# Optimization experiments

Measured on AMD Instinct MI355X. Metric: run time of the kernel, lower is better.

The kernel has to match this reference:

```python
import jax, jax.numpy as jnp
import numpy as np


def _pano_affinity():
    # Faithful port of get_pano_affinity(): 3 rings of 12 views, 3x3 Gaussian
    # blur (cv2 ksize=3 sigma=0 => sigma=0.8), BORDER_TRANSPARENT (borders kept),
    # diagonal reset to 1; zeros replaced by 0.01 as done in __init__.
    p = np.eye(36, dtype=np.float64)
    for v in range(12):  # top ring
        p[v, v + 12] = 1
        l = (v - 1) % 12
        r = (v + 1) % 12
        p[v, l] = 1; p[v, l + 12] = 1
        p[v, r] = 1; p[v, r + 12] = 1
    for v in range(12, 24):  # middle ring
        p[v, v + 12] = 1; p[v, v - 12] = 1
        l = (v - 13) % 12 + 12
        r = (v - 11) % 12 + 12
        p[v, l] = 1; p[v, l + 12] = 1; p[v, l - 12] = 1
        p[v, r] = 1; p[v, r + 12] = 1; p[v, r - 12] = 1
    for v in range(24, 36):  # bottom ring
        p[v, v - 12] = 1
        l = (v - 25) % 12 + 24
        r = (v - 23) % 12 + 24
        p[v, l] = 1; p[v, l - 12] = 1
        p[v, r] = 1; p[v, r - 12] = 1
    assert np.sum(p - p.T) == 0
    kern = np.exp(-np.array([-1.0, 0.0, 1.0]) ** 2 / (2 * 0.8 ** 2))
    kern /= kern.sum()
    a, b = kern[0], kern[1]
    t = a * p[:, :-2] + b * p[:, 1:-1] + a * p[:, 2:]
    t2 = a * t[:-2, :] + b * t[1:-1, :] + a * t[2:, :]
    out = p.copy()
    out[1:-1, 1:-1] = t2  # transparent border: edge pixels unblurred
    out[np.eye(36, dtype=bool)] = 1.0
    out[out == 0] = 0.01
    return out.astype(np.float32)


def _ln(x, g, b):
    mu = jnp.mean(x, -1, keepdims=True)
    v = jnp.mean(jnp.square(x - mu), -1, keepdims=True)
    return (x - mu) * jax.lax.rsqrt(v + 1e-5) * g + b


def setup_inputs() -> dict:
    key = jax.random.key(0)
    ks = jax.random.split(key, 12)
    B, L, V, D, KD, KV, Q, H = 128, 36, 36, 512, 300, 112, 36, 512
    s = 0.02
    return {
        'h': jax.random.normal(ks[0], (B, Q), jnp.float32),
        'context': jax.random.normal(ks[1], (B, L, V, D), jnp.float32),
        'teacher_action_view_ids': jax.random.randint(ks[2], (B,), 0, 36),
        'detect_feats': jax.random.normal(ks[3], (B, L, KD), jnp.float32),
        'knowledge_vector': jax.random.normal(ks[4], (B, L, KV), jnp.float32),
        'pano_a': jnp.asarray(_pano_affinity()),
        'W_q': jax.random.normal(ks[5], (Q, Q), jnp.float32) * s,
        'W_k': jax.random.normal(ks[6], (Q, D + KD), jnp.float32) * s,
        'gru_Wih': jax.random.normal(ks[7], (3 * Q, D + KV), jnp.float32) * s,
        'gru_Whh': jax.random.normal(ks[8], (3 * Q, Q), jnp.float32) * s,
        'gru_bih': jnp.zeros((3 * Q,), jnp.float32),
        'gru_bhh': jnp.zeros((3 * Q,), jnp.float32),
        'ln_slots_g': jnp.ones((Q,), jnp.float32),
        'ln_slots_b': jnp.zeros((Q,), jnp.float32),
        'ln_ff_g': jnp.ones((Q,), jnp.float32),
        'ln_ff_b': jnp.zeros((Q,), jnp.float32),
        'mlp_W1': jax.random.normal(ks[9], (H, Q), jnp.float32) * s,
        'mlp_b1': jnp.zeros((H,), jnp.float32),
        'mlp_W2': jax.random.normal(ks[10], (Q, H), jnp.float32) * s,
        'mlp_b2': jnp.zeros((Q,), jnp.float32),
    }


def reference(h, context, teacher_action_view_ids, detect_feats, knowledge_vector,
              pano_a, W_q, W_k, gru_Wih, gru_Whh, gru_bih, gru_bhh,
              ln_slots_g, ln_slots_b, ln_ff_g, ln_ff_b,
              mlp_W1, mlp_b1, mlp_W2, mlp_b2):
    B, L, V, D = context.shape
    Q = pano_a.shape[0]  # 36
    scale = Q ** -0.5
    iters = 3
    slots = jnp.broadcast_to(pano_a, (B, Q, Q))
    # context_know = cat(context, detect_feats broadcast over 36 views)
    ck = jnp.concatenate(
        [context, jnp.broadcast_to(detect_feats[:, :, None, :], (B, L, V, detect_feats.shape[-1]))], axis=-1)
    k = jnp.einsum('bljc,qc->bljq', ck, W_k)  # [B,L,36,Q]
    attn_ws = []
    for _ in range(iters):
        slots_prev = slots
        q = jnp.einsum('bie,qe->biq', _ln(slots, ln_slots_g, ln_slots_b), W_q)  # [B,Q,Q]
        dots = jnp.einsum('bid,bkjd->bkj', q, k) * scale  # i summed out, as in source
        attn = jax.nn.softmax(dots, axis=-1)  # softmax over views
        attn_ws.append(attn)
        updates = jnp.einsum('bkjd,bij->bid', context, attn)  # [B,L,D]
        x = jnp.concatenate([updates, knowledge_vector], axis=-1).reshape(-1, D + knowledge_vector.shape[-1])
        hp = slots_prev.reshape(-1, Q)
        # torch.nn.GRUCell (gate order r, z, n)
        gx = x @ gru_Wih.T + gru_bih
        gh = hp @ gru_Whh.T + gru_bhh
        xr, xz, xn = jnp.split(gx, 3, axis=-1)
        hr, hz, hn = jnp.split(gh, 3, axis=-1)
        r = jax.nn.sigmoid(xr + hr)
        z = jax.nn.sigmoid(xz + hz)
        n = jnp.tanh(xn + r * hn)
        gnew = ((1.0 - z) * n + z * hp).reshape(B, -1, Q)
        ff = _ln(gnew, ln_ff_g, ln_ff_b)
        gnew = gnew + (jax.nn.relu(ff @ mlp_W1.T + mlp_b1) @ mlp_W2.T + mlp_b2)
        slots = gnew
    return slots, jnp.stack(attn_ws, 0)
```

## Files before the change

### kernel.cpp

```cpp
#include <hip/hip_runtime.h>

namespace {
constexpr int Bc = 128, Lc = 36, Vc = 36, Dc = 512, KDc = 300, KVc = 112, Qc = 36, Hc = 512;
constexpr int ROWS = Bc * Lc * Vc;
constexpr int BLn  = Bc * Lc;
constexpr int SLOT = Bc * Qc * Qc;
constexpr float SCALE = 1.0f / 6.0f;
}

__device__ __forceinline__ float wave_sum(float v) {
  #pragma unroll
  for (int off = 32; off > 0; off >>= 1) v += __shfl_xor(v, off, 64);
  return v;
}
__device__ __forceinline__ float wave_max(float v) {
  #pragma unroll
  for (int off = 32; off > 0; off >>= 1) v = fmaxf(v, __shfl_xor(v, off, 64));
  return v;
}
__device__ __forceinline__ float sigmoidf_(float x) { return 1.f / (1.f + __expf(-x)); }
__device__ __forceinline__ float dot4_(float4 a, float4 b) {
  return fmaf(a.x, b.x, fmaf(a.y, b.y, fmaf(a.z, b.z, a.w * b.w)));
}

__global__ __launch_bounds__(256) void csum_kernel(const float* __restrict__ ctx, float* __restrict__ csum) {
  int tid = blockIdx.x * 256 + threadIdx.x;
  int b  = tid / (Vc * Dc);
  int jd = tid % (Vc * Dc);
  const float* p = ctx + (size_t)b * Lc * Vc * Dc + jd;
  float s = 0.f;
  #pragma unroll
  for (int l = 0; l < Lc; ++l) s += p[(size_t)l * (Vc * Dc)];
  csum[tid] = s;
}

__global__ void kd_kernel(const float* __restrict__ det, const float* __restrict__ Wk,
                          float* __restrict__ kd) {
  __shared__ float ds[KDc];
  int bl = blockIdx.x; int t = threadIdx.x;
  for (int c = t; c < KDc; c += 64) ds[c] = det[(size_t)bl * KDc + c];
  __syncthreads();
  if (t < Qc) {
    const float* w = Wk + (size_t)t * 812 + 512;
    float acc = 0.f;
    #pragma unroll 4
    for (int c = 0; c < KDc; ++c) acc = fmaf(ds[c], w[c], acc);
    kd[(size_t)bl * Qc + t] = acc;
  }
}

__global__ __launch_bounds__(256) void k_gemm(const float* __restrict__ A, const float* __restrict__ Wk,
                       const float* __restrict__ kd, float* __restrict__ kout) {
  __shared__ __align__(16) float As[32 * 260];
  __shared__ __align__(16) float Bs[32 * 48];
  int t = threadIdx.x;
  int rb = blockIdx.x * 256;
  int tr = t & 63, tc = t >> 6;
  float acc[4][9];
  #pragma unroll
  for (int i = 0; i < 4; ++i)
    #pragma unroll
    for (int c = 0; c < 9; ++c) acc[i][c] = 0.f;

  for (int d0 = 0; d0 < 512; d0 += 32) {
    #pragma unroll
    for (int jj = 0; jj < 8; ++jj) {
      int idx = t + jj * 256;
      int kkb = (idx & 7) * 4, r = idx >> 3;
      const float4 v = *(const float4*)(A + (size_t)(rb + r) * 512 + d0 + kkb);
      As[(kkb + 0) * 260 + r] = v.x;
      As[(kkb + 1) * 260 + r] = v.y;
      As[(kkb + 2) * 260 + r] = v.z;
      As[(kkb + 3) * 260 + r] = v.w;
    }
    for (int idx = t; idx < 32 * 36; idx += 256) {
      int kk = idx / 36, c = idx % 36;
      Bs[kk * 48 + (c / 9) * 12 + (c % 9)] = Wk[(size_t)c * 812 + d0 + kk];
    }
    __syncthreads();
    #pragma unroll
    for (int kk = 0; kk < 32; ++kk) {
      const float4 a  = *(const float4*)&As[kk * 260 + tr * 4];
      const float* bp = &Bs[kk * 48 + tc * 12];
      const float4 b0 = *(const float4*)bp;
      const float4 b1 = *(const float4*)(bp + 4);
      const float  b8 = bp[8];
      const float av[4] = {a.x, a.y, a.z, a.w};
      const float bv[9] = {b0.x, b0.y, b0.z, b0.w, b1.x, b1.y, b1.z, b1.w, b8};
      #pragma unroll
      for (int i = 0; i < 4; ++i)
        #pragma unroll
        for (int c = 0; c < 9; ++c) acc[i][c] = fmaf(av[i], bv[c], acc[i][c]);
    }
    __syncthreads();
  }
  #pragma unroll
  for (int i = 0; i < 4; ++i) {
    int row = rb + tr * 4 + i;
    int bl = row / 36;
    #pragma unroll
    for (int c = 0; c < 9; ++c) {
      int q = tc * 9 + c;
      kout[(size_t)row * 36 + q] = acc[i][c] + kd[(size_t)bl * 36 + q];
    }
  }
}

__global__ __launch_bounds__(256) void prew_gemm(const float* __restrict__ A, int lda, int K, int k0,
                                                 const float* __restrict__ Wih, float* __restrict__ outp) {
  __shared__ __align__(16) float As[16 * 68];
  __shared__ __align__(16) float Bs[16 * 112];
  int t = threadIdx.x;
  int rb = blockIdx.x * 64;
  int tr = t & 63, tc = t >> 6;
  float acc[27];
  #pragma unroll
  for (int c = 0; c < 27; ++c) acc[c] = 0.f;

  for (int kk0 = 0; kk0 < K; kk0 += 16) {
    {
      int r = t >> 2, kq = (t & 3) * 4;
      const float4 v = *(const float4*)(A + (size_t)(rb + r) * lda + kk0 + kq);
      As[(kq + 0) * 68 + r] = v.x;
      As[(kq + 1) * 68 + r] = v.y;
      As[(kq + 2) * 68 + r] = v.z;
      As[(kq + 3) * 68 + r] = v.w;
    }
    for (int idx = t; idx < 16 * 108; idx += 256) {
      int k = idx / 108, c = idx % 108;
      Bs[k * 112 + (c / 27) * 28 + (c % 27)] = Wih[(size_t)c * 624 + k0 + kk0 + k];
    }
    __syncthreads();
    #pragma unroll
    for (int k = 0; k < 16; ++k) {
      const float a = As[k * 68 + tr];
      const float* bp = &Bs[k * 112 + tc * 28];
      float bv[27];
      #pragma unroll
      for (int c4 = 0; c4 < 6; ++c4) {
        float4 b4 = *(const float4*)(bp + c4 * 4);
        bv[c4 * 4 + 0] = b4.x; bv[c4 * 4 + 1] = b4.y; bv[c4 * 4 + 2] = b4.z; bv[c4 * 4 + 3] = b4.w;
      }
      bv[24] = bp[24]; bv[25] = bp[25]; bv[26] = bp[26];
      #pragma unroll
      for (int c = 0; c < 27; ++c) acc[c] = fmaf(a, bv[c], acc[c]);
    }
    __syncthreads();
  }
  int row = rb + tr;
  #pragma unroll
  for (int c = 0; c < 27; ++c)
    outp[(size_t)row * 108 + tc * 27 + c] = acc[c];
}

__global__ __launch_bounds__(512) void mega_kernel(
    const float* __restrict__ pano, const float* __restrict__ kmat,
    const float* __restrict__ cw,   const float* __restrict__ gknw,
    const float* __restrict__ Wq,   const float* __restrict__ Whh,
    const float* __restrict__ bih,  const float* __restrict__ bhh,
    const float* __restrict__ lsg,  const float* __restrict__ lsb,
    const float* __restrict__ lfg,  const float* __restrict__ lfb,
    const float* __restrict__ W1,   const float* __restrict__ b1,
    const float* __restrict__ W2,   const float* __restrict__ b2,
    float* __restrict__ out) {
  const int b = blockIdx.x;
  const int t = threadIdx.x;
  const int wv = t >> 6, lane = t & 63;

  __shared__ __align__(16) float s0[36 * 40], s1[36 * 40];
  __shared__ float at[36 * 36];
  __shared__ __align__(16) float cw_s[36 * 108], gk_s[36 * 108];
  __shared__ __align__(16) float whh_s[108 * 44];
  __shared__ __align__(16) float ff_s[36 * 40];
  __shared__ float ls8[8 * 37];
  __shared__ float qs[36];
  __shared__ __align__(16) float mid_s[36 * 132];

  for (int q4 = t; q4 < 972; q4 += 512) {
    *(float4*)&cw_s[q4 * 4] = *(const float4*)(cw   + (size_t)b * 3888 + q4 * 4);
    *(float4*)&gk_s[q4 * 4] = *(const float4*)(gknw + (size_t)b * 3888 + q4 * 4);
  }
  for (int idx = t; idx < 3888; idx += 512)
    whh_s[(idx / 36) * 44 + idx % 36] = Whh[idx];
  for (int idx = t; idx < 1296; idx += 512)
    s0[(idx / 36) * 40 + idx % 36] = pano[idx];
  float gv = 0.f, bv = 0.f, fg = 0.f, fb = 0.f, b2v = 0.f;
  if (lane < 36) { gv = lsg[lane]; bv = lsb[lane]; fg = lfg[lane]; fb = lfb[lane]; b2v = b2[lane]; }
  const float* kb = kmat + (size_t)b * 1296 * 36;
  __syncthreads();

  for (int it = 0; it < 3; ++it) {
    float* cur = (it == 1) ? s1 : s0;
    float* nxt = (it == 1) ? s0 : s1;
    float* aout = out + SLOT + (size_t)it * SLOT + (size_t)b * 1296;

    float lnsum = 0.f;
    #pragma unroll
    for (int ii = 0; ii < 5; ++ii) {
      int i = wv + 8 * ii;
      bool act = (i < 36) && (lane < 36);
      float x = act ? cur[i * 40 + lane] : 0.f;
      float mu = wave_sum(x) * (1.f / 36.f);
      float d = x - mu;
      float var = wave_sum(act ? d * d : 0.f) * (1.f / 36.f);
      float ln = d * rsqrtf(var + 1e-5f) * gv + bv;
      if (act) lnsum += ln;
    }
    if (lane < 36) ls8[wv * 37 + lane] = lnsum;
    __syncthreads();
    if (t < 36) {
      float l0 = 0.f;
      #pragma unroll
      for (int w = 0; w < 8; ++w) l0 += ls8[w * 37 + t];
      ls8[8 * 37 - 37 + t] = 0.f;
      float acc = 0.f;
      ls8[296 - 296 + t] = l0;
    }
    __syncthreads();
    if (t < 36) {
      float acc = 0.f;
      #pragma unroll
      for (int e = 0; e < 36; ++e) acc = fmaf(ls8[e], Wq[t * 36 + e], acc);
      qs[t] = acc;
    }
    __syncthreads();

    #pragma unroll
    for (int ii = 0; ii < 5; ++ii) {
      int l = wv + 8 * ii;
      if (l < 36) {
        float dot = 0.f;
        if (lane < 36) {
          const float* kp = kb + ((size_t)l * 36 + lane) * 36;
          #pragma unroll
          for (int c = 0; c < 9; ++c) {
            float4 kv = *(const float4*)(kp + 4 * c);
            dot += kv.x * qs[4 * c] + kv.y * qs[4 * c + 1] + kv.z * qs[4 * c + 2] + kv.w * qs[4 * c + 3];
          }
        }
        dot *= SCALE;
        float m = wave_max((lane < 36) ? dot : -1e30f);
        float e = (lane < 36) ? __expf(dot - m) : 0.f;
        float s = wave_sum(e);
        if (lane < 36) {
          float a = e / s;
          at[l * 36 + lane] = a;
          aout[(size_t)l * 36 + lane] = a;
        }
      }
    }
    __syncthreads();

    if (t < 324) {
      int i0 = (t / 18) * 2, c0 = (t % 18) * 2;
      float ax[3][2][2], ah[3][2][2];
      #pragma unroll
      for (int g = 0; g < 3; ++g)
        #pragma unroll
        for (int r = 0; r < 2; ++r)
          #pragma unroll
          for (int cc = 0; cc < 2; ++cc) {
            ax[g][r][cc] = gk_s[(i0 + r) * 108 + g * 36 + c0 + cc] + bih[g * 36 + c0 + cc];
            ah[g][r][cc] = bhh[g * 36 + c0 + cc];
          }
      #pragma unroll 4
      for (int j = 0; j < 36; ++j) {
        float a0 = at[i0 * 36 + j], a1 = at[(i0 + 1) * 36 + j];
        #pragma unroll
        for (int g = 0; g < 3; ++g)
          #pragma unroll
          for (int cc = 0; cc < 2; ++cc) {
            float wjc = cw_s[j * 108 + g * 36 + c0 + cc];
            ax[g][0][cc] = fmaf(a0, wjc, ax[g][0][cc]);
            ax[g][1][cc] = fmaf(a1, wjc, ax[g][1][cc]);
          }
      }
      #pragma unroll
      for (int eq = 0; eq < 9; ++eq) {
        float4 h0q = *(const float4*)&cur[i0 * 40 + eq * 4];
        float4 h1q = *(const float4*)&cur[(i0 + 1) * 40 + eq * 4];
        #pragma unroll
        for (int g = 0; g < 3; ++g)
          #pragma unroll
          for (int cc = 0; cc < 2; ++cc) {
            float4 wq4 = *(const float4*)&whh_s[(g * 36 + c0 + cc) * 44 + eq * 4];
            ah[g][0][cc] += dot4_(h0q, wq4);
            ah[g][1][cc] += dot4_(h1q, wq4);
          }
      }
      #pragma unroll
      for (int r = 0; r < 2; ++r)
        #pragma unroll
        for (int cc = 0; cc < 2; ++cc) {
          int i = i0 + r, c = c0 + cc;
          float hp = cur[i * 40 + c];
          float rr = sigmoidf_(ax[0][r][cc] + ah[0][r][cc]);
          float zz = sigmoidf_(ax[1][r][cc] + ah[1][r][cc]);
          float nn = tanhf(ax[2][r][cc] + rr * ah[2][r][cc]);
          nxt[i * 40 + c] = (1.f - zz) * nn + zz * hp;
        }
    }
    __syncthreads();

    #pragma unroll
    for (int ii = 0; ii < 5; ++ii) {
      int i = wv + 8 * ii;
      if (i < 36) {
        float v = (lane < 36) ? nxt[i * 40 + lane] : 0.f;
        float mu = wave_sum(v) * (1.f / 36.f);
        float d = v - mu;
        float var = wave_sum((lane < 36) ? d * d : 0.f) * (1.f / 36.f);
        float rstd = rsqrtf(var + 1e-5f);
        if (lane < 36) {
          ff_s[i * 40 + lane] = d * rstd * fg + fb;
          nxt[i * 40 + lane] = v + b2v;
        }
      }
    }
    __syncthreads();

    float acc2[2][2] = {{0.f, 0.f}, {0.f, 0.f}};
    for (int h0 = 0; h0 < 512; h0 += 128) {
      if (t < 384) {
        int ig = t >> 5, hq = t & 31;
        int i_0 = ig * 3;
        int hh = h0 + hq * 4;
        float4 bq = *(const float4*)&b1[hh];
        float m[3][4] = {{bq.x, bq.y, bq.z, bq.w},
                         {bq.x, bq.y, bq.z, bq.w},
                         {bq.x, bq.y, bq.z, bq.w}};
        const float* w1p = W1 + (size_t)hh * 36;
        #pragma unroll
        for (int eq = 0; eq < 9; ++eq) {
          float4 f0 = *(const float4*)&ff_s[i_0 * 40 + eq * 4];
          float4 f1 = *(const float4*)&ff_s[(i_0 + 1) * 40 + eq * 4];
          float4 f2 = *(const float4*)&ff_s[(i_0 + 2) * 40 + eq * 4];
          #pragma unroll
          for (int c = 0; c < 4; ++c) {
            float4 wq4 = *(const float4*)(w1p + (size_t)c * 36 + eq * 4);
            m[0][c] += dot4_(f0, wq4);
            m[1][c] += dot4_(f1, wq4);
            m[2][c] += dot4_(f2, wq4);
          }
        }
        #pragma unroll
        for (int r = 0; r < 3; ++r) {
          float4 o;
          o.x = fmaxf(m[r][0], 0.f); o.y = fmaxf(m[r][1], 0.f);
          o.z = fmaxf(m[r][2], 0.f); o.w = fmaxf(m[r][3], 0.f);
          *(float4*)&mid_s[(i_0 + r) * 132 + hq * 4] = o;
        }
      }
      __syncthreads();
      if (t < 324) {
        int i0 = (t / 18) * 2, c0 = (t % 18) * 2;
        const float* w2a = W2 + (size_t)c0 * 512 + h0;
        const float* w2b = W2 + (size_t)(c0 + 1) * 512 + h0;
        #pragma unroll 8
        for (int kq = 0; kq < 32; ++kq) {
          float4 m0 = *(const float4*)&mid_s[i0 * 132 + kq * 4];
          float4 m1 = *(const float4*)&mid_s[(i0 + 1) * 132 + kq * 4];
          float4 w0 = *(const float4*)(w2a + kq * 4);
          float4 w1 = *(const float4*)(w2b + kq * 4);
          acc2[0][0] += dot4_(m0, w0);
          acc2[0][1] += dot4_(m0, w1);
          acc2[1][0] += dot4_(m1, w0);
          acc2[1][1] += dot4_(m1, w1);
        }
      }
      __syncthreads();
    }
    if (t < 324) {
      int i0 = (t / 18) * 2, c0 = (t % 18) * 2;
      nxt[i0 * 40 + c0]             += acc2[0][0];
      nxt[i0 * 40 + c0 + 1]         += acc2[0][1];
      nxt[(i0 + 1) * 40 + c0]       += acc2[1][0];
      nxt[(i0 + 1) * 40 + c0 + 1]   += acc2[1][1];
    }
    __syncthreads();
  }

  for (int v4 = t; v4 < 324; v4 += 512) {
    int row = v4 / 9, q = v4 % 9;
    *(float4*)&out[(size_t)b * 1296 + row * 36 + q * 4] = *(const float4*)&s1[row * 40 + q * 4];
  }
}

extern "C" void kernel_launch(void* const* d_in, const int* in_sizes, int n_in,
                              void* d_out, int out_size, void* d_ws, size_t ws_size,
                              hipStream_t stream) {
  const float* ctx  = (const float*)d_in[1];
  const float* det  = (const float*)d_in[3];
  const float* knw  = (const float*)d_in[4];
  const float* pano = (const float*)d_in[5];
  const float* Wq   = (const float*)d_in[6];
  const float* Wk   = (const float*)d_in[7];
  const float* Wih  = (const float*)d_in[8];
  const float* Whh  = (const float*)d_in[9];
  const float* bih  = (const float*)d_in[10];
  const float* bhh  = (const float*)d_in[11];
  const float* lsg  = (const float*)d_in[12];
  const float* lsb  = (const float*)d_in[13];
  const float* lfg  = (const float*)d_in[14];
  const float* lfb  = (const float*)d_in[15];
  const float* W1   = (const float*)d_in[16];
  const float* b1   = (const float*)d_in[17];
  const float* W2   = (const float*)d_in[18];
  const float* b2   = (const float*)d_in[19];
  float* out = (float*)d_out;

  float* w = (float*)d_ws;
  float* kmat = w; w += (size_t)ROWS * 36;
  float* csum = w; w += (size_t)Bc * Vc * Dc;
  float* kd   = w; w += (size_t)BLn * Qc;
  float* cw   = w; w += (size_t)BLn * 108;
  float* gknw = w; w += (size_t)BLn * 108;

  csum_kernel<<<(Bc * Vc * Dc) / 256, 256, 0, stream>>>(ctx, csum);
  kd_kernel<<<BLn, 64, 0, stream>>>(det, Wk, kd);
  k_gemm<<<ROWS / 256, 256, 0, stream>>>(ctx, Wk, kd, kmat);
  prew_gemm<<<72, 256, 0, stream>>>(csum, 512, 512, 0,   Wih, cw);
  prew_gemm<<<72, 256, 0, stream>>>(knw,  112, 112, 512, Wih, gknw);
  mega_kernel<<<Bc, 512, 0, stream>>>(pano, kmat, cw, gknw, Wq, Whh, bih, bhh,
                                      lsg, lsb, lfg, lfb, W1, b1, W2, b2, out);
}
```

Baseline: 1.104 ms.

## Transpose K matrix layout and widen mega_kernel to 1024 threads

k_gemm now writes the key matrix transposed ([B,Q,L*V]), so the per-iteration dots in mega_kernel become coalesced column reads into a shared dots buffer. The softmax then runs from that buffer. mega_kernel doubles to 1024 threads with smaller per-thread tiles in the GRU and MLP stages, and caches the biases in shared memory. The scattered transposed stores in k_gemm may cost more, and the larger block raises register pressure. The mega kernel uses only 128 blocks, so more threads per block is meant to hide latency.

```diff
diff --git a/kernel.cpp b/kernel.cpp
--- a/kernel.cpp
+++ b/kernel.cpp
@@ -97,11 +97,13 @@
   #pragma unroll
   for (int i = 0; i < 4; ++i) {
     int row = rb + tr * 4 + i;
+    int bq = row / 1296;
+    int lj = row % 1296;
     int bl = row / 36;
     #pragma unroll
     for (int c = 0; c < 9; ++c) {
       int q = tc * 9 + c;
-      kout[(size_t)row * 36 + q] = acc[i][c] + kd[(size_t)bl * 36 + q];
+      kout[((size_t)bq * 36 + q) * 1296 + lj] = acc[i][c] + kd[(size_t)bl * 36 + q];
     }
   }
 }
@@ -153,8 +155,8 @@
     outp[(size_t)row * 108 + tc * 27 + c] = acc[c];
 }
 
-__global__ __launch_bounds__(512) void mega_kernel(
-    const float* __restrict__ pano, const float* __restrict__ kmat,
+__global__ __launch_bounds__(1024) void mega_kernel(
+    const float* __restrict__ pano, const float* __restrict__ kmatT,
     const float* __restrict__ cw,   const float* __restrict__ gknw,
     const float* __restrict__ Wq,   const float* __restrict__ Whh,
     const float* __restrict__ bih,  const float* __restrict__ bhh,
@@ -169,24 +171,30 @@
 
   __shared__ __align__(16) float s0[36 * 40], s1[36 * 40];
   __shared__ float at[36 * 36];
+  __shared__ float dt_s[36 * 36];
   __shared__ __align__(16) float cw_s[36 * 108], gk_s[36 * 108];
   __shared__ __align__(16) float whh_s[108 * 44];
   __shared__ __align__(16) float ff_s[36 * 40];
-  __shared__ float ls8[8 * 37];
+  __shared__ float ls16[16 * 37];
+  __shared__ float qred[36];
   __shared__ float qs[36];
   __shared__ __align__(16) float mid_s[36 * 132];
-
-  for (int q4 = t; q4 < 972; q4 += 512) {
+  __shared__ __align__(16) float b1_s[512];
+  __shared__ float bih_s[108], bhh_s[108];
+
+  for (int q4 = t; q4 < 972; q4 += 1024) {
     *(float4*)&cw_s[q4 * 4] = *(const float4*)(cw   + (size_t)b * 3888 + q4 * 4);
     *(float4*)&gk_s[q4 * 4] = *(const float4*)(gknw + (size_t)b * 3888 + q4 * 4);
   }
-  for (int idx = t; idx < 3888; idx += 512)
+  for (int idx = t; idx < 3888; idx += 1024)
     whh_s[(idx / 36) * 44 + idx % 36] = Whh[idx];
-  for (int idx = t; idx < 1296; idx += 512)
+  for (int idx = t; idx < 1296; idx += 1024)
     s0[(idx / 36) * 40 + idx % 36] = pano[idx];
+  if (t < 512) b1_s[t] = b1[t];
+  if (t < 108) { bih_s[t] = bih[t]; bhh_s[t] = bhh[t]; }
   float gv = 0.f, bv = 0.f, fg = 0.f, fb = 0.f, b2v = 0.f;
   if (lane < 36) { gv = lsg[lane]; bv = lsb[lane]; fg = lfg[lane]; fb = lfb[lane]; b2v = b2[lane]; }
-  const float* kb = kmat + (size_t)b * 1296 * 36;
+  const float* kbT = kmatT + (size_t)b * 36 * 1296;
   __syncthreads();
 
   for (int it = 0; it < 3; ++it) {
@@ -196,51 +204,47 @@
 
     float lnsum = 0.f;
     #pragma unroll
-    for (int ii = 0; ii < 5; ++ii) {
-      int i = wv + 8 * ii;
+    for (int ii = 0; ii < 3; ++ii) {
+      int i = wv + 16 * ii;
       bool act = (i < 36) && (lane < 36);
       float x = act ? cur[i * 40 + lane] : 0.f;
       float mu = wave_sum(x) * (1.f / 36.f);
       float d = x - mu;
       float var = wave_sum(act ? d * d : 0.f) * (1.f / 36.f);
-      float ln = d * rsqrtf(var + 1e-5f) * gv + bv;
-      if (act) lnsum += ln;
-    }
-    if (lane < 36) ls8[wv * 37 + lane] = lnsum;
+      if (act) lnsum += d * rsqrtf(var + 1e-5f) * gv + bv;
+    }
+    if (lane < 36) ls16[wv * 37 + lane] = lnsum;
     __syncthreads();
     if (t < 36) {
       float l0 = 0.f;
       #pragma unroll
-      for (int w = 0; w < 8; ++w) l0 += ls8[w * 37 + t];
-      ls8[8 * 37 - 37 + t] = 0.f;
-      float acc = 0.f;
-      ls8[296 - 296 + t] = l0;
+      for (int w = 0; w < 16; ++w) l0 += ls16[w * 37 + t];
+      qred[t] = l0;
     }
     __syncthreads();
     if (t < 36) {
       float acc = 0.f;
-      #pragma unroll
-      for (int e = 0; e < 36; ++e) acc = fmaf(ls8[e], Wq[t * 36 + e], acc);
+      #pragma unroll 9
+      for (int e = 0; e < 36; ++e) acc = fmaf(qred[e], Wq[t * 36 + e], acc);
       qs[t] = acc;
     }
     __syncthreads();
 
-    #pragma unroll
-    for (int ii = 0; ii < 5; ++ii) {
-      int l = wv + 8 * ii;
+    for (int lj = t; lj < 1296; lj += 1024) {
+      const float* kp = kbT + lj;
+      float acc = 0.f;
+      #pragma unroll 9
+      for (int q = 0; q < 36; ++q) acc = fmaf(kp[(size_t)q * 1296], qs[q], acc);
+      dt_s[lj] = acc * SCALE;
+    }
+    __syncthreads();
+    #pragma unroll
+    for (int ii = 0; ii < 3; ++ii) {
+      int l = wv + 16 * ii;
       if (l < 36) {
-        float dot = 0.f;
-        if (lane < 36) {
-          const float* kp = kb + ((size_t)l * 36 + lane) * 36;
-          #pragma unroll
-          for (int c = 0; c < 9; ++c) {
-            float4 kv = *(const float4*)(kp + 4 * c);
-            dot += kv.x * qs[4 * c] + kv.y * qs[4 * c + 1] + kv.z * qs[4 * c + 2] + kv.w * qs[4 * c + 3];
-          }
-        }
-        dot *= SCALE;
-        float m = wave_max((lane < 36) ? dot : -1e30f);
-        float e = (lane < 36) ? __expf(dot - m) : 0.f;
+        float dv = (lane < 36) ? dt_s[l * 36 + lane] : -1e30f;
+        float m = wave_max(dv);
+        float e = (lane < 36) ? __expf(dv - m) : 0.f;
         float s = wave_sum(e);
         if (lane < 36) {
           float a = e / s;
@@ -251,60 +255,49 @@
     }
     __syncthreads();
 
-    if (t < 324) {
-      int i0 = (t / 18) * 2, c0 = (t % 18) * 2;
-      float ax[3][2][2], ah[3][2][2];
+    if (t < 648) {
+      int i = t / 18, c0 = (t % 18) * 2;
+      float ax[3][2], ah[3][2];
       #pragma unroll
       for (int g = 0; g < 3; ++g)
         #pragma unroll
-        for (int r = 0; r < 2; ++r)
-          #pragma unroll
-          for (int cc = 0; cc < 2; ++cc) {
-            ax[g][r][cc] = gk_s[(i0 + r) * 108 + g * 36 + c0 + cc] + bih[g * 36 + c0 + cc];
-            ah[g][r][cc] = bhh[g * 36 + c0 + cc];
-          }
-      #pragma unroll 4
+        for (int cc = 0; cc < 2; ++cc) {
+          ax[g][cc] = gk_s[i * 108 + g * 36 + c0 + cc] + bih_s[g * 36 + c0 + cc];
+          ah[g][cc] = bhh_s[g * 36 + c0 + cc];
+        }
+      #pragma unroll 6
       for (int j = 0; j < 36; ++j) {
-        float a0 = at[i0 * 36 + j], a1 = at[(i0 + 1) * 36 + j];
+        float a0 = at[i * 36 + j];
         #pragma unroll
         for (int g = 0; g < 3; ++g)
           #pragma unroll
-          for (int cc = 0; cc < 2; ++cc) {
-            float wjc = cw_s[j * 108 + g * 36 + c0 + cc];
-            ax[g][0][cc] = fmaf(a0, wjc, ax[g][0][cc]);
-            ax[g][1][cc] = fmaf(a1, wjc, ax[g][1][cc]);
-          }
+          for (int cc = 0; cc < 2; ++cc)
+            ax[g][cc] = fmaf(a0, cw_s[j * 108 + g * 36 + c0 + cc], ax[g][cc]);
       }
       #pragma unroll
       for (int eq = 0; eq < 9; ++eq) {
-        float4 h0q = *(const float4*)&cur[i0 * 40 + eq * 4];
-        float4 h1q = *(const float4*)&cur[(i0 + 1) * 40 + eq * 4];
+        float4 hq = *(const float4*)&cur[i * 40 + eq * 4];
         #pragma unroll
         for (int g = 0; g < 3; ++g)
           #pragma unroll
-          for (int cc = 0; cc < 2; ++cc) {
-            float4 wq4 = *(const float4*)&whh_s[(g * 36 + c0 + cc) * 44 + eq * 4];
-            ah[g][0][cc] += dot4_(h0q, wq4);
-            ah[g][1][cc] += dot4_(h1q, wq4);
-          }
-      }
-      #pragma unroll
-      for (int r = 0; r < 2; ++r)
-        #pragma unroll
-        for (int cc = 0; cc < 2; ++cc) {
-          int i = i0 + r, c = c0 + cc;
-          float hp = cur[i * 40 + c];
-          float rr = sigmoidf_(ax[0][r][cc] + ah[0][r][cc]);
-          float zz = sigmoidf_(ax[1][r][cc] + ah[1][r][cc]);
-          float nn = tanhf(ax[2][r][cc] + rr * ah[2][r][cc]);
-          nxt[i * 40 + c] = (1.f - zz) * nn + zz * hp;
-        }
-    }
-    __syncthreads();
-
-    #pragma unroll
-    for (int ii = 0; ii < 5; ++ii) {
-      int i = wv + 8 * ii;
+          for (int cc = 0; cc < 2; ++cc)
+            ah[g][cc] += dot4_(hq, *(const float4*)&whh_s[(g * 36 + c0 + cc) * 44 + eq * 4]);
+      }
+      #pragma unroll
+      for (int cc = 0; cc < 2; ++cc) {
+        int c = c0 + cc;
+        float hp = cur[i * 40 + c];
+        float rr = sigmoidf_(ax[0][cc] + ah[0][cc]);
+        float zz = sigmoidf_(ax[1][cc] + ah[1][cc]);
+        float nn = tanhf(ax[2][cc] + rr * ah[2][cc]);
+        nxt[i * 40 + c] = (1.f - zz) * nn + zz * hp;
+      }
+    }
+    __syncthreads();
+
+    #pragma unroll
+    for (int ii = 0; ii < 3; ++ii) {
+      int i = wv + 16 * ii;
       if (i < 36) {
         float v = (lane < 36) ? nxt[i * 40 + lane] : 0.f;
         float mu = wave_sum(v) * (1.f / 36.f);
@@ -319,68 +312,56 @@
     }
     __syncthreads();
 
-    float acc2[2][2] = {{0.f, 0.f}, {0.f, 0.f}};
+    float acc2[2] = {0.f, 0.f};
     for (int h0 = 0; h0 < 512; h0 += 128) {
-      if (t < 384) {
-        int ig = t >> 5, hq = t & 31;
-        int i_0 = ig * 3;
+      if (t < 576) {
+        int i0 = (t >> 5) * 2, hq = t & 31;
         int hh = h0 + hq * 4;
-        float4 bq = *(const float4*)&b1[hh];
-        float m[3][4] = {{bq.x, bq.y, bq.z, bq.w},
-                         {bq.x, bq.y, bq.z, bq.w},
-                         {bq.x, bq.y, bq.z, bq.w}};
+        float4 bq = *(const float4*)&b1_s[hh];
+        float m[2][4] = {{bq.x, bq.y, bq.z, bq.w}, {bq.x, bq.y, bq.z, bq.w}};
         const float* w1p = W1 + (size_t)hh * 36;
         #pragma unroll
         for (int eq = 0; eq < 9; ++eq) {
-          float4 f0 = *(const float4*)&ff_s[i_0 * 40 + eq * 4];
-          float4 f1 = *(const float4*)&ff_s[(i_0 + 1) * 40 + eq * 4];
-          float4 f2 = *(const float4*)&ff_s[(i_0 + 2) * 40 + eq * 4];
+          float4 f0 = *(const float4*)&ff_s[i0 * 40 + eq * 4];
+          float4 f1 = *(const float4*)&ff_s[(i0 + 1) * 40 + eq * 4];
           #pragma unroll
           for (int c = 0; c < 4; ++c) {
             float4 wq4 = *(const float4*)(w1p + (size_t)c * 36 + eq * 4);
             m[0][c] += dot4_(f0, wq4);
             m[1][c] += dot4_(f1, wq4);
-            m[2][c] += dot4_(f2, wq4);
           }
         }
         #pragma unroll
-        for (int r = 0; r < 3; ++r) {
+        for (int r = 0; r < 2; ++r) {
           float4 o;
           o.x = fmaxf(m[r][0], 0.f); o.y = fmaxf(m[r][1], 0.f);
           o.z = fmaxf(m[r][2], 0.f); o.w = fmaxf(m[r][3], 0.f);
-          *(float4*)&mid_s[(i_0 + r) * 132 + hq * 4] = o;
+          *(float4*)&mid_s[(i0 + r) * 132 + hq * 4] = o;
         }
       }
       __syncthreads();
-      if (t < 324) {
-        int i0 = (t / 18) * 2, c0 = (t % 18) * 2;
+      if (t < 648) {
+        int i = t / 18, c0 = (t % 18) * 2;
         const float* w2a = W2 + (size_t)c0 * 512 + h0;
-        const float* w2b = W2 + (size_t)(c0 + 1) * 512 + h0;
+        const float* w2b = w2a + 512;
         #pragma unroll 8
         for (int kq = 0; kq < 32; ++kq) {
-          float4 m0 = *(const float4*)&mid_s[i0 * 132 + kq * 4];
-          float4 m1 = *(const float4*)&mid_s[(i0 + 1) * 132 + kq * 4];
-          float4 w0 = *(const float4*)(w2a + kq * 4);
-          float4 w1 = *(const float4*)(w2b + kq * 4);
-          acc2[0][0] += dot4_(m0, w0);
-          acc2[0][1] += dot4_(m0, w1);
-          acc2[1][0] += dot4_(m1, w0);
-          acc2[1][1] += dot4_(m1, w1);
+          float4 mm = *(const float4*)&mid_s[i * 132 + kq * 4];
+          acc2[0] += dot4_(mm, *(const float4*)(w2a + kq * 4));
+          acc2[1] += dot4_(mm, *(const float4*)(w2b + kq * 4));
         }
       }
       __syncthreads();
     }
-    if (t < 324) {
-      int i0 = (t / 18) * 2, c0 = (t % 18) * 2;
-      nxt[i0 * 40 + c0]             += acc2[0][0];
-      nxt[i0 * 40 + c0 + 1]         += acc2[0][1];
-      nxt[(i0 + 1) * 40 + c0]       += acc2[1][0];
-      nxt[(i0 + 1) * 40 + c0 + 1]   += acc2[1][1];
-    }
-    __syncthreads();
-  }
-
-  for (int v4 = t; v4 < 324; v4 += 512) {
+    if (t < 648) {
+      int i = t / 18, c0 = (t % 18) * 2;
+      nxt[i * 40 + c0]     += acc2[0];
+      nxt[i * 40 + c0 + 1] += acc2[1];
+    }
+    __syncthreads();
+  }
+
+  for (int v4 = t; v4 < 324; v4 += 1024) {
     int row = v4 / 9, q = v4 % 9;
     *(float4*)&out[(size_t)b * 1296 + row * 36 + q * 4] = *(const float4*)&s1[row * 40 + q * 4];
   }
@@ -410,17 +391,17 @@
   float* out = (float*)d_out;
 
   float* w = (float*)d_ws;
-  float* kmat = w; w += (size_t)ROWS * 36;
-  float* csum = w; w += (size_t)Bc * Vc * Dc;
-  float* kd   = w; w += (size_t)BLn * Qc;
-  float* cw   = w; w += (size_t)BLn * 108;
-  float* gknw = w; w += (size_t)BLn * 108;
+  float* kmatT = w; w += (size_t)ROWS * 36;
+  float* csum  = w; w += (size_t)Bc * Vc * Dc;
+  float* kd    = w; w += (size_t)BLn * Qc;
+  float* cw    = w; w += (size_t)BLn * 108;
+  float* gknw  = w; w += (size_t)BLn * 108;
 
   csum_kernel<<<(Bc * Vc * Dc) / 256, 256, 0, stream>>>(ctx, csum);
   kd_kernel<<<BLn, 64, 0, stream>>>(det, Wk, kd);
-  k_gemm<<<ROWS / 256, 256, 0, stream>>>(ctx, Wk, kd, kmat);
+  k_gemm<<<ROWS / 256, 256, 0, stream>>>(ctx, Wk, kd, kmatT);
   prew_gemm<<<72, 256, 0, stream>>>(csum, 512, 512, 0,   Wih, cw);
   prew_gemm<<<72, 256, 0, stream>>>(knw,  112, 112, 512, Wih, gknw);
-  mega_kernel<<<Bc, 512, 0, stream>>>(pano, kmat, cw, gknw, Wq, Whh, bih, bhh,
-                                      lsg, lsb, lfg, lfb, W1, b1, W2, b2, out);
-}
+  mega_kernel<<<Bc, 1024, 0, stream>>>(pano, kmatT, cw, gknw, Wq, Whh, bih, bhh,
+                                       lsg, lsb, lfg, lfb, W1, b1, W2, b2, out);
+}
```

After: 1.266 ms. +14.7%, slower.
